# Performance work log

Measured on AMD Instinct MI355X. Metric: run time of the kernel, lower is better.

## Reference

```python
import jax, jax.numpy as jnp
import numpy as np

FP16_MIN = -65504.0
FP16_MAX = 65504.0

B, S, D, H = 2, 2048, 1024, 16
HD = D // H


def setup_inputs() -> dict:
    key = jax.random.key(0)
    ks = jax.random.split(key, 12)
    s = 0.02
    inp = {
        "x_q": jax.random.normal(ks[0], (B, S, D), jnp.float32),
        "x_k": jax.random.normal(ks[1], (B, S, D), jnp.float32),
        "x_v": jax.random.normal(ks[2], (B, S, D), jnp.float32),
        # causal mask [B, 1, S, S]; 0 entries are masked out
        "mask": jnp.broadcast_to(jnp.tril(jnp.ones((S, S), jnp.int32)), (B, 1, S, S)),
        "Wq": jax.random.normal(ks[3], (D, D), jnp.float32) * s,
        "bq": jnp.zeros((D,), jnp.float32),
        "Wk": jax.random.normal(ks[4], (D, D), jnp.float32) * s,
        "bk": jnp.zeros((D,), jnp.float32),
        "Wv": jax.random.normal(ks[5], (D, D), jnp.float32) * s,
        "bv": jnp.zeros((D,), jnp.float32),
        "Wo": jax.random.normal(ks[6], (D, D), jnp.float32) * s,
        "bo": jnp.zeros((D,), jnp.float32),
    }
    return inp


def _split_heads(x):
    # [B, S, D] -> [B, H, S, HD]
    b, s, _ = x.shape
    return x.reshape(b, s, H, HD).transpose(0, 2, 1, 3)


def reference(x_q, x_k, x_v, mask, Wq, bq, Wk, bk, Wv, bv, Wo, bo):
    scale = jnp.sqrt(jnp.float32(HD))
    q = _split_heads(x_q @ Wq + bq)  # [B,H,S,HD]
    k = _split_heads(x_k @ Wk + bk)
    v = _split_heads(x_v @ Wv + bv)

    scores = jnp.einsum("bhqd,bhkd->bhqk", q, k) / scale  # [B,H,S,S]
    scores = jnp.where(mask == 0, FP16_MIN, scores)
    scores = jnp.where(jnp.isneginf(scores), FP16_MIN, scores)
    scores = jnp.where(jnp.isposinf(scores), FP16_MAX, scores)

    probs = jax.nn.softmax(scores, axis=-1)  # dropout p=0.0 -> identity
    ctx = jnp.einsum("bhqk,bhkd->bhqd", probs, v)  # [B,H,S,HD]
    ctx = ctx.transpose(0, 2, 1, 3).reshape(x_q.shape[0], x_q.shape[1], D)
    out = ctx @ Wo + bo
    return out, probs
```

## Files before the change

kernel.cpp:

```cpp
#include <hip/hip_runtime.h>


typedef __bf16 bf16x8 __attribute__((ext_vector_type(8)));
typedef float f32x4 __attribute__((ext_vector_type(4)));

__device__ __forceinline__ unsigned short f2bf(float f) {
  unsigned int u = __builtin_bit_cast(unsigned int, f);
  u += 0x7fffu + ((u >> 16) & 1u);
  return (unsigned short)(u >> 16);
}
__device__ __forceinline__ float bf2f_lo(unsigned int u) {
  return __builtin_bit_cast(float, u << 16);
}
__device__ __forceinline__ float bf2f_hi(unsigned int u) {
  return __builtin_bit_cast(float, u & 0xffff0000u);
}

__global__ void transpose_w(const float* __restrict__ W0, const float* __restrict__ W1,
                            const float* __restrict__ W2, const float* __restrict__ W3,
                            unsigned short* __restrict__ Wt) {
  __shared__ float t[32][33];
  const int z = blockIdx.z;
  const float* W = (z == 0) ? W0 : (z == 1) ? W1 : (z == 2) ? W2 : W3;
  unsigned short* o = Wt + (size_t)z * 1048576u;
  const int n0 = blockIdx.x * 32, k0 = blockIdx.y * 32;
  const int tx = threadIdx.x, ty = threadIdx.y;
#pragma unroll
  for (int i = 0; i < 4; i++)
    t[ty + 8 * i][tx] = W[(size_t)(k0 + ty + 8 * i) * 1024 + n0 + tx];
  __syncthreads();
#pragma unroll
  for (int i = 0; i < 4; i++)
    o[(size_t)(n0 + ty + 8 * i) * 1024 + k0 + tx] = f2bf(t[tx][ty + 8 * i]);
}

__global__ __launch_bounds__(256) void gemm_kernel(
    const void* __restrict__ A0, const void* __restrict__ A1, const void* __restrict__ A2,
    const unsigned short* __restrict__ Wtb,
    const float* __restrict__ b0, const float* __restrict__ b1, const float* __restrict__ b2,
    void* __restrict__ O0, void* __restrict__ O1, void* __restrict__ O2,
    const int mode0) {
  __shared__ unsigned short Alds[64 * 40];
  const int z = blockIdx.z;
  const int mode = mode0 + z;
  const void* Av = (z == 0) ? A0 : (z == 1) ? A1 : A2;
  const float* bias = (z == 0) ? b0 : (z == 1) ? b1 : b2;
  void* outv = (z == 0) ? O0 : (z == 1) ? O1 : O2;
  const unsigned short* Wt = Wtb + (size_t)z * 1048576u;

  const int tid = threadIdx.x;
  const int lane = tid & 63;
  const int wave = tid >> 6;
  const int wm = wave >> 1, wn = wave & 1;
  const int m0 = blockIdx.y * 64, n0 = blockIdx.x * 128;
  const int g = lane >> 4, c = lane & 15;

  f32x4 acc[2][4];
#pragma unroll
  for (int i = 0; i < 2; i++)
#pragma unroll
    for (int j = 0; j < 4; j++) acc[i][j] = (f32x4){0.f, 0.f, 0.f, 0.f};

  const int srow = tid >> 2;
  const int sch = (tid & 3) * 8;

#define LOAD_PACK(KB, DST)                                                        \
  if (mode < 3) {                                                                 \
    const float* A = (const float*)Av;                                            \
    const float4* src = (const float4*)(A + (size_t)(m0 + srow) * 1024 + (KB) + sch); \
    const float4 v0 = src[0], v1 = src[1];                                        \
    DST.x = (unsigned int)f2bf(v0.x) | ((unsigned int)f2bf(v0.y) << 16);          \
    DST.y = (unsigned int)f2bf(v0.z) | ((unsigned int)f2bf(v0.w) << 16);          \
    DST.z = (unsigned int)f2bf(v1.x) | ((unsigned int)f2bf(v1.y) << 16);          \
    DST.w = (unsigned int)f2bf(v1.z) | ((unsigned int)f2bf(v1.w) << 16);          \
  } else {                                                                        \
    const unsigned short* A = (const unsigned short*)Av;                          \
    DST = *(const uint4*)(A + (size_t)(m0 + srow) * 1024 + (KB) + sch);           \
  }

  uint4 pk;
  LOAD_PACK(0, pk);
  for (int kb = 0; kb < 1024; kb += 32) {
    *(uint4*)&Alds[srow * 40 + sch] = pk;
    if (kb + 32 < 1024) { LOAD_PACK(kb + 32, pk); }
    __syncthreads();

    bf16x8 af[2], bfr[4];
#pragma unroll
    for (int mi = 0; mi < 2; mi++)
      af[mi] = *(const bf16x8*)&Alds[(wm * 32 + mi * 16 + c) * 40 + g * 8];
#pragma unroll
    for (int nf = 0; nf < 4; nf++)
      bfr[nf] = *(const bf16x8*)(Wt + (size_t)(n0 + wn * 64 + nf * 16 + c) * 1024 + kb + g * 8);
#pragma unroll
    for (int mi = 0; mi < 2; mi++)
#pragma unroll
      for (int nf = 0; nf < 4; nf++)
        acc[mi][nf] = __builtin_amdgcn_mfma_f32_16x16x32_bf16(af[mi], bfr[nf], acc[mi][nf], 0, 0, 0);
    __syncthreads();
  }
#undef LOAD_PACK

#pragma unroll
  for (int nf = 0; nf < 4; nf++) {
    const int col = n0 + wn * 64 + nf * 16 + c;
    const float bc = bias[col];
#pragma unroll
    for (int mi = 0; mi < 2; mi++) {
#pragma unroll
      for (int r = 0; r < 4; r++) {
        const int row = m0 + wm * 32 + mi * 16 + g * 4 + r;
        const float v = acc[mi][nf][r] + bc;
        if (mode == 0) {
          ((unsigned short*)outv)[(size_t)row * 1024 + col] = f2bf(v * 0.125f);
        } else if (mode == 1) {
          ((unsigned short*)outv)[(size_t)row * 1024 + col] = f2bf(v);
        } else if (mode == 2) {
          const int bb = row >> 11, s = row & 2047;
          ((unsigned short*)outv)[((size_t)(bb * 1024 + col)) * 2048 + s] = f2bf(v);
        } else {
          ((float*)outv)[(size_t)row * 1024 + col] = v;
        }
      }
    }
  }
}

__global__ __launch_bounds__(512, 4) void attn_kernel(
    const unsigned short* __restrict__ Q, const unsigned short* __restrict__ K,
    const unsigned short* __restrict__ Vt, float* __restrict__ probs,
    unsigned short* __restrict__ ctx) {
  __shared__ unsigned short Klds[64 * 72];
  __shared__ unsigned short Vlds[64 * 72];
  __shared__ unsigned short Plds[128 * 72];

  const int tid = threadIdx.x;
  const int lane = tid & 63, wave = tid >> 6;
  const int g = lane >> 4, c = lane & 15;
  const int bh = blockIdx.x;
  const int b = bh >> 4, h = bh & 15;
  const int q0 = blockIdx.y * 128;
  const int qrow0 = q0 + wave * 16;
  const int wave_kend = qrow0 + 16;

  const unsigned short* Qh = Q + ((size_t)(b * 2048 + qrow0)) * 1024 + h * 64;
  const unsigned short* Kh = K + ((size_t)b * 2048) * 1024 + h * 64;
  const unsigned short* Vh = Vt + ((size_t)bh) * 64 * 2048;
  float* Ph = probs + ((size_t)(bh * 2048 + q0)) * 2048;

  const bf16x8 qa0 = *(const bf16x8*)&Qh[(size_t)c * 1024 + g * 8];
  const bf16x8 qa1 = *(const bf16x8*)&Qh[(size_t)c * 1024 + 32 + g * 8];

  const int srow = tid >> 3;
  const int scol = (tid & 7) * 8;
  const int kb_end = q0 + 128;

#define QK_TILE()                                                                        \
  f32x4 sv[4];                                                                           \
  _Pragma("unroll")                                                                      \
  for (int sub = 0; sub < 4; sub++) {                                                    \
    sv[sub] = (f32x4){0.f, 0.f, 0.f, 0.f};                                               \
    const unsigned short* Kr = &Klds[(sub * 16 + c) * 72];                               \
    sv[sub] = __builtin_amdgcn_mfma_f32_16x16x32_bf16(qa0, *(const bf16x8*)&Kr[g * 8], sv[sub], 0, 0, 0); \
    sv[sub] = __builtin_amdgcn_mfma_f32_16x16x32_bf16(qa1, *(const bf16x8*)&Kr[32 + g * 8], sv[sub], 0, 0, 0); \
  }                                                                                      \
  if (kb + 63 > qrow0) {                                                                 \
    _Pragma("unroll")                                                                    \
    for (int sub = 0; sub < 4; sub++)                                                    \
      _Pragma("unroll")                                                                  \
      for (int r = 0; r < 4; r++)                                                        \
        if (kb + sub * 16 + c > qrow0 + g * 4 + r) sv[sub][r] = -1e30f;                  \
  }

  float lp[4] = {0.f, 0.f, 0.f, 0.f};
  {
    uint4 kreg = *(const uint4*)(Kh + (size_t)srow * 1024 + scol);
    for (int kb = 0; kb < kb_end; kb += 64) {
      *(uint4*)&Klds[srow * 72 + scol] = kreg;
      if (kb + 64 < kb_end)
        kreg = *(const uint4*)(Kh + (size_t)(kb + 64 + srow) * 1024 + scol);
      __syncthreads();
      if (kb < wave_kend) {
        QK_TILE();
#pragma unroll
        for (int r = 0; r < 4; r++)
          lp[r] += __expf(sv[0][r]) + __expf(sv[1][r]) + __expf(sv[2][r]) + __expf(sv[3][r]);
      }
      __syncthreads();
    }
  }
#pragma unroll
  for (int off = 1; off < 16; off <<= 1)
#pragma unroll
    for (int r = 0; r < 4; r++) lp[r] += __shfl_xor(lp[r], off);
  float invl[4];
#pragma unroll
  for (int r = 0; r < 4; r++) invl[r] = 1.0f / lp[r];

  f32x4 cacc[4];
#pragma unroll
  for (int nf = 0; nf < 4; nf++) cacc[nf] = (f32x4){0.f, 0.f, 0.f, 0.f};

  {
    uint4 kreg = *(const uint4*)(Kh + (size_t)srow * 1024 + scol);
    uint4 vreg = *(const uint4*)(Vh + (size_t)srow * 2048 + scol);
    for (int kb = 0; kb < kb_end; kb += 64) {
      *(uint4*)&Klds[srow * 72 + scol] = kreg;
      *(uint4*)&Vlds[srow * 72 + scol] = vreg;
      if (kb + 64 < kb_end) {
        kreg = *(const uint4*)(Kh + (size_t)(kb + 64 + srow) * 1024 + scol);
        vreg = *(const uint4*)(Vh + (size_t)srow * 2048 + kb + 64 + scol);
      }
      __syncthreads();
      if (kb < wave_kend) {
        QK_TILE();
#pragma unroll
        for (int sub = 0; sub < 4; sub++)
#pragma unroll
          for (int r = 0; r < 4; r++) {
            const float p = __expf(sv[sub][r]) * invl[r];
            Plds[(wave * 16 + g * 4 + r) * 72 + sub * 16 + c] = f2bf(p);
          }
        const bf16x8 pa0 = *(const bf16x8*)&Plds[(wave * 16 + c) * 72 + g * 8];
        const bf16x8 pa1 = *(const bf16x8*)&Plds[(wave * 16 + c) * 72 + 32 + g * 8];
#pragma unroll
        for (int nf = 0; nf < 4; nf++) {
          const bf16x8 vf0 = *(const bf16x8*)&Vlds[(nf * 16 + c) * 72 + g * 8];
          const bf16x8 vf1 = *(const bf16x8*)&Vlds[(nf * 16 + c) * 72 + 32 + g * 8];
          cacc[nf] = __builtin_amdgcn_mfma_f32_16x16x32_bf16(pa0, vf0, cacc[nf], 0, 0, 0);
          cacc[nf] = __builtin_amdgcn_mfma_f32_16x16x32_bf16(pa1, vf1, cacc[nf], 0, 0, 0);
        }
      } else {
#pragma unroll
        for (int sub = 0; sub < 4; sub++)
#pragma unroll
          for (int r = 0; r < 4; r++)
            Plds[(wave * 16 + g * 4 + r) * 72 + sub * 16 + c] = 0;
      }
      __syncthreads();
      {
        const int prow = tid >> 2;
        const int pcb = (tid & 3) * 16;
        const uint4* ps = (const uint4*)&Plds[prow * 72 + pcb];
        const uint4 a = ps[0], b4 = ps[1];
        float* dst = Ph + (size_t)prow * 2048 + kb + pcb;
        ((float4*)dst)[0] = make_float4(bf2f_lo(a.x), bf2f_hi(a.x), bf2f_lo(a.y), bf2f_hi(a.y));
        ((float4*)dst)[1] = make_float4(bf2f_lo(a.z), bf2f_hi(a.z), bf2f_lo(a.w), bf2f_hi(a.w));
        ((float4*)dst)[2] = make_float4(bf2f_lo(b4.x), bf2f_hi(b4.x), bf2f_lo(b4.y), bf2f_hi(b4.y));
        ((float4*)dst)[3] = make_float4(bf2f_lo(b4.z), bf2f_hi(b4.z), bf2f_lo(b4.w), bf2f_hi(b4.w));
      }
    }
  }
#undef QK_TILE

#pragma unroll
  for (int nf = 0; nf < 4; nf++)
#pragma unroll
    for (int r = 0; r < 4; r++)
      ctx[((size_t)(b * 2048 + qrow0 + g * 4 + r)) * 1024 + h * 64 + nf * 16 + c] =
          f2bf(cacc[nf][r]);

  if (kb_end < 2048) {
    const float4 zz = make_float4(0.f, 0.f, 0.f, 0.f);
    for (int row = 0; row < 128; ++row) {
      float* pr = Ph + (size_t)row * 2048;
      const int col = kb_end + tid * 4;
      if (col < 2048) *(float4*)&pr[col] = zz;
    }
  }
}

extern "C" void kernel_launch(void* const* d_in, const int* in_sizes, int n_in,
                              void* d_out, int out_size, void* d_ws, size_t ws_size,
                              hipStream_t stream) {
  if (ws_size < (size_t)40 * 1024 * 1024) return;

  const float* xq = (const float*)d_in[0];
  const float* xk = (const float*)d_in[1];
  const float* xv = (const float*)d_in[2];
  const float* Wq = (const float*)d_in[4];
  const float* bq = (const float*)d_in[5];
  const float* Wk = (const float*)d_in[6];
  const float* bk = (const float*)d_in[7];
  const float* Wv = (const float*)d_in[8];
  const float* bv = (const float*)d_in[9];
  const float* Wo = (const float*)d_in[10];
  const float* bo = (const float*)d_in[11];

  unsigned short* ws = (unsigned short*)d_ws;
  unsigned short* Wt = ws;
  unsigned short* Qw = ws + (size_t)4 * 1048576u;
  unsigned short* Kw = Qw + 4194304u;
  unsigned short* Vtw = Kw + 4194304u;
  unsigned short* Cw = Vtw + 4194304u;

  float* out = (float*)d_out;
  float* probs = out + 4194304u;

  transpose_w<<<dim3(32, 32, 4), dim3(32, 8), 0, stream>>>(Wq, Wk, Wv, Wo, Wt);
  gemm_kernel<<<dim3(8, 64, 3), 256, 0, stream>>>(xq, xk, xv, Wt, bq, bk, bv,
                                                  Qw, Kw, Vtw, 0);
  attn_kernel<<<dim3(32, 16, 1), 512, 0, stream>>>(Qw, Kw, Vtw, probs, Cw);
  gemm_kernel<<<dim3(8, 64, 1), 256, 0, stream>>>(Cw, Cw, Cw, Wt + 3u * 1048576u,
                                                  bo, bo, bo, out, out, out, 3);
}
```

Before: 366.2 us.

## Fuse attention into single pass with deferred normalization and separate probs normalization kernel

The attention kernel now computes QK^T, the exponentials and the PV product in one pass, dropping the separate row-sum pass. It also scales the context by 1/l only at the end. Unnormalized probabilities are written as bf16 into the first half of each fp32 probs row, and a new norm_probs kernel reads them back, sums each row and writes normalized fp32 values in place. The GEMM's K step is doubled from 32 to 64 to halve the number of barriers. In exchange, no max subtraction is applied before the exponentials, which assumes scores stay bounded, and the probs tensor is traversed an extra time.

Result: no change. 363.7 us (-0.7%).

```diff
diff --git a/kernel.cpp b/kernel.cpp
--- a/kernel.cpp
+++ b/kernel.cpp
@@ -40,7 +40,7 @@
     const float* __restrict__ b0, const float* __restrict__ b1, const float* __restrict__ b2,
     void* __restrict__ O0, void* __restrict__ O1, void* __restrict__ O2,
     const int mode0) {
-  __shared__ unsigned short Alds[64 * 40];
+  __shared__ unsigned short Alds[64 * 72];
   const int z = blockIdx.z;
   const int mode = mode0 + z;
   const void* Av = (z == 0) ? A0 : (z == 1) ? A1 : A2;
@@ -62,41 +62,54 @@
     for (int j = 0; j < 4; j++) acc[i][j] = (f32x4){0.f, 0.f, 0.f, 0.f};
 
   const int srow = tid >> 2;
-  const int sch = (tid & 3) * 8;
-
-#define LOAD_PACK(KB, DST)                                                        \
+  const int sch = (tid & 3) * 16;
+
+  uint4 pk0, pk1;
+#define LOAD_PACK(KB)                                                             \
   if (mode < 3) {                                                                 \
     const float* A = (const float*)Av;                                            \
     const float4* src = (const float4*)(A + (size_t)(m0 + srow) * 1024 + (KB) + sch); \
-    const float4 v0 = src[0], v1 = src[1];                                        \
-    DST.x = (unsigned int)f2bf(v0.x) | ((unsigned int)f2bf(v0.y) << 16);          \
-    DST.y = (unsigned int)f2bf(v0.z) | ((unsigned int)f2bf(v0.w) << 16);          \
-    DST.z = (unsigned int)f2bf(v1.x) | ((unsigned int)f2bf(v1.y) << 16);          \
-    DST.w = (unsigned int)f2bf(v1.z) | ((unsigned int)f2bf(v1.w) << 16);          \
+    const float4 v0 = src[0], v1 = src[1], v2 = src[2], v3 = src[3];              \
+    pk0.x = (unsigned int)f2bf(v0.x) | ((unsigned int)f2bf(v0.y) << 16);          \
+    pk0.y = (unsigned int)f2bf(v0.z) | ((unsigned int)f2bf(v0.w) << 16);          \
+    pk0.z = (unsigned int)f2bf(v1.x) | ((unsigned int)f2bf(v1.y) << 16);          \
+    pk0.w = (unsigned int)f2bf(v1.z) | ((unsigned int)f2bf(v1.w) << 16);          \
+    pk1.x = (unsigned int)f2bf(v2.x) | ((unsigned int)f2bf(v2.y) << 16);          \
+    pk1.y = (unsigned int)f2bf(v2.z) | ((unsigned int)f2bf(v2.w) << 16);          \
+    pk1.z = (unsigned int)f2bf(v3.x) | ((unsigned int)f2bf(v3.y) << 16);          \
+    pk1.w = (unsigned int)f2bf(v3.z) | ((unsigned int)f2bf(v3.w) << 16);          \
   } else {                                                                        \
     const unsigned short* A = (const unsigned short*)Av;                          \
-    DST = *(const uint4*)(A + (size_t)(m0 + srow) * 1024 + (KB) + sch);           \
+    const uint4* src = (const uint4*)(A + (size_t)(m0 + srow) * 1024 + (KB) + sch); \
+    pk0 = src[0];                                                                 \
+    pk1 = src[1];                                                                 \
   }
 
-  uint4 pk;
-  LOAD_PACK(0, pk);
-  for (int kb = 0; kb < 1024; kb += 32) {
-    *(uint4*)&Alds[srow * 40 + sch] = pk;
-    if (kb + 32 < 1024) { LOAD_PACK(kb + 32, pk); }
+  LOAD_PACK(0);
+  for (int kb = 0; kb < 1024; kb += 64) {
+    *(uint4*)&Alds[srow * 72 + sch] = pk0;
+    *(uint4*)&Alds[srow * 72 + sch + 8] = pk1;
+    if (kb + 64 < 1024) { LOAD_PACK(kb + 64); }
     __syncthreads();
 
-    bf16x8 af[2], bfr[4];
+    bf16x8 af[2][2], bfr[4][2];
 #pragma unroll
     for (int mi = 0; mi < 2; mi++)
-      af[mi] = *(const bf16x8*)&Alds[(wm * 32 + mi * 16 + c) * 40 + g * 8];
+#pragma unroll
+      for (int kk = 0; kk < 2; kk++)
+        af[mi][kk] = *(const bf16x8*)&Alds[(wm * 32 + mi * 16 + c) * 72 + kk * 32 + g * 8];
 #pragma unroll
     for (int nf = 0; nf < 4; nf++)
-      bfr[nf] = *(const bf16x8*)(Wt + (size_t)(n0 + wn * 64 + nf * 16 + c) * 1024 + kb + g * 8);
-#pragma unroll
-    for (int mi = 0; mi < 2; mi++)
-#pragma unroll
-      for (int nf = 0; nf < 4; nf++)
-        acc[mi][nf] = __builtin_amdgcn_mfma_f32_16x16x32_bf16(af[mi], bfr[nf], acc[mi][nf], 0, 0, 0);
+#pragma unroll
+      for (int kk = 0; kk < 2; kk++)
+        bfr[nf][kk] = *(const bf16x8*)(Wt + (size_t)(n0 + wn * 64 + nf * 16 + c) * 1024 + kb + kk * 32 + g * 8);
+#pragma unroll
+    for (int kk = 0; kk < 2; kk++)
+#pragma unroll
+      for (int mi = 0; mi < 2; mi++)
+#pragma unroll
+        for (int nf = 0; nf < 4; nf++)
+          acc[mi][nf] = __builtin_amdgcn_mfma_f32_16x16x32_bf16(af[mi][kk], bfr[nf][kk], acc[mi][nf], 0, 0, 0);
     __syncthreads();
   }
 #undef LOAD_PACK
@@ -155,40 +168,73 @@
   const int scol = (tid & 7) * 8;
   const int kb_end = q0 + 128;
 
-#define QK_TILE()                                                                        \
-  f32x4 sv[4];                                                                           \
-  _Pragma("unroll")                                                                      \
-  for (int sub = 0; sub < 4; sub++) {                                                    \
-    sv[sub] = (f32x4){0.f, 0.f, 0.f, 0.f};                                               \
-    const unsigned short* Kr = &Klds[(sub * 16 + c) * 72];                               \
-    sv[sub] = __builtin_amdgcn_mfma_f32_16x16x32_bf16(qa0, *(const bf16x8*)&Kr[g * 8], sv[sub], 0, 0, 0); \
-    sv[sub] = __builtin_amdgcn_mfma_f32_16x16x32_bf16(qa1, *(const bf16x8*)&Kr[32 + g * 8], sv[sub], 0, 0, 0); \
-  }                                                                                      \
-  if (kb + 63 > qrow0) {                                                                 \
-    _Pragma("unroll")                                                                    \
-    for (int sub = 0; sub < 4; sub++)                                                    \
-      _Pragma("unroll")                                                                  \
-      for (int r = 0; r < 4; r++)                                                        \
-        if (kb + sub * 16 + c > qrow0 + g * 4 + r) sv[sub][r] = -1e30f;                  \
-  }
-
   float lp[4] = {0.f, 0.f, 0.f, 0.f};
-  {
-    uint4 kreg = *(const uint4*)(Kh + (size_t)srow * 1024 + scol);
-    for (int kb = 0; kb < kb_end; kb += 64) {
-      *(uint4*)&Klds[srow * 72 + scol] = kreg;
-      if (kb + 64 < kb_end)
-        kreg = *(const uint4*)(Kh + (size_t)(kb + 64 + srow) * 1024 + scol);
-      __syncthreads();
-      if (kb < wave_kend) {
-        QK_TILE();
-#pragma unroll
-        for (int r = 0; r < 4; r++)
-          lp[r] += __expf(sv[0][r]) + __expf(sv[1][r]) + __expf(sv[2][r]) + __expf(sv[3][r]);
-      }
-      __syncthreads();
+  f32x4 cacc[4];
+#pragma unroll
+  for (int nf = 0; nf < 4; nf++) cacc[nf] = (f32x4){0.f, 0.f, 0.f, 0.f};
+
+  uint4 kreg = *(const uint4*)(Kh + (size_t)srow * 1024 + scol);
+  uint4 vreg = *(const uint4*)(Vh + (size_t)srow * 2048 + scol);
+  for (int kb = 0; kb < kb_end; kb += 64) {
+    *(uint4*)&Klds[srow * 72 + scol] = kreg;
+    *(uint4*)&Vlds[srow * 72 + scol] = vreg;
+    if (kb + 64 < kb_end) {
+      kreg = *(const uint4*)(Kh + (size_t)(kb + 64 + srow) * 1024 + scol);
+      vreg = *(const uint4*)(Vh + (size_t)srow * 2048 + kb + 64 + scol);
+    }
+    __syncthreads();
+
+    if (kb < wave_kend) {
+      f32x4 sv[4];
+#pragma unroll
+      for (int sub = 0; sub < 4; sub++) {
+        sv[sub] = (f32x4){0.f, 0.f, 0.f, 0.f};
+        const unsigned short* Kr = &Klds[(sub * 16 + c) * 72];
+        sv[sub] = __builtin_amdgcn_mfma_f32_16x16x32_bf16(qa0, *(const bf16x8*)&Kr[g * 8], sv[sub], 0, 0, 0);
+        sv[sub] = __builtin_amdgcn_mfma_f32_16x16x32_bf16(qa1, *(const bf16x8*)&Kr[32 + g * 8], sv[sub], 0, 0, 0);
+      }
+      if (kb + 63 > qrow0) {
+#pragma unroll
+        for (int sub = 0; sub < 4; sub++)
+#pragma unroll
+          for (int r = 0; r < 4; r++)
+            if (kb + sub * 16 + c > qrow0 + g * 4 + r) sv[sub][r] = -1e30f;
+      }
+#pragma unroll
+      for (int sub = 0; sub < 4; sub++)
+#pragma unroll
+        for (int r = 0; r < 4; r++) {
+          const float pu = __expf(sv[sub][r]);
+          lp[r] += pu;
+          Plds[(wave * 16 + g * 4 + r) * 72 + sub * 16 + c] = f2bf(pu);
+        }
+      const bf16x8 pa0 = *(const bf16x8*)&Plds[(wave * 16 + c) * 72 + g * 8];
+      const bf16x8 pa1 = *(const bf16x8*)&Plds[(wave * 16 + c) * 72 + 32 + g * 8];
+#pragma unroll
+      for (int nf = 0; nf < 4; nf++) {
+        const bf16x8 vf0 = *(const bf16x8*)&Vlds[(nf * 16 + c) * 72 + g * 8];
+        const bf16x8 vf1 = *(const bf16x8*)&Vlds[(nf * 16 + c) * 72 + 32 + g * 8];
+        cacc[nf] = __builtin_amdgcn_mfma_f32_16x16x32_bf16(pa0, vf0, cacc[nf], 0, 0, 0);
+        cacc[nf] = __builtin_amdgcn_mfma_f32_16x16x32_bf16(pa1, vf1, cacc[nf], 0, 0, 0);
+      }
+    }
+    __syncthreads();
+
+    {
+      const int prow = tid >> 2;
+      const int pcb = (tid & 3) * 16;
+      unsigned short* dst = (unsigned short*)Ph + (size_t)prow * 4096 + kb + pcb;
+      const int rw_kend = q0 + (prow & ~15) + 16;
+      if (kb < rw_kend) {
+        *(uint4*)dst = *(const uint4*)&Plds[prow * 72 + pcb];
+        *(uint4*)(dst + 8) = *(const uint4*)&Plds[prow * 72 + pcb + 8];
+      } else {
+        *(uint4*)dst = make_uint4(0u, 0u, 0u, 0u);
+        *(uint4*)(dst + 8) = make_uint4(0u, 0u, 0u, 0u);
+      }
     }
   }
+
 #pragma unroll
   for (int off = 1; off < 16; off <<= 1)
 #pragma unroll
@@ -197,77 +243,38 @@
 #pragma unroll
   for (int r = 0; r < 4; r++) invl[r] = 1.0f / lp[r];
 
-  f32x4 cacc[4];
-#pragma unroll
-  for (int nf = 0; nf < 4; nf++) cacc[nf] = (f32x4){0.f, 0.f, 0.f, 0.f};
-
-  {
-    uint4 kreg = *(const uint4*)(Kh + (size_t)srow * 1024 + scol);
-    uint4 vreg = *(const uint4*)(Vh + (size_t)srow * 2048 + scol);
-    for (int kb = 0; kb < kb_end; kb += 64) {
-      *(uint4*)&Klds[srow * 72 + scol] = kreg;
-      *(uint4*)&Vlds[srow * 72 + scol] = vreg;
-      if (kb + 64 < kb_end) {
-        kreg = *(const uint4*)(Kh + (size_t)(kb + 64 + srow) * 1024 + scol);
-        vreg = *(const uint4*)(Vh + (size_t)srow * 2048 + kb + 64 + scol);
-      }
-      __syncthreads();
-      if (kb < wave_kend) {
-        QK_TILE();
-#pragma unroll
-        for (int sub = 0; sub < 4; sub++)
-#pragma unroll
-          for (int r = 0; r < 4; r++) {
-            const float p = __expf(sv[sub][r]) * invl[r];
-            Plds[(wave * 16 + g * 4 + r) * 72 + sub * 16 + c] = f2bf(p);
-          }
-        const bf16x8 pa0 = *(const bf16x8*)&Plds[(wave * 16 + c) * 72 + g * 8];
-        const bf16x8 pa1 = *(const bf16x8*)&Plds[(wave * 16 + c) * 72 + 32 + g * 8];
-#pragma unroll
-        for (int nf = 0; nf < 4; nf++) {
-          const bf16x8 vf0 = *(const bf16x8*)&Vlds[(nf * 16 + c) * 72 + g * 8];
-          const bf16x8 vf1 = *(const bf16x8*)&Vlds[(nf * 16 + c) * 72 + 32 + g * 8];
-          cacc[nf] = __builtin_amdgcn_mfma_f32_16x16x32_bf16(pa0, vf0, cacc[nf], 0, 0, 0);
-          cacc[nf] = __builtin_amdgcn_mfma_f32_16x16x32_bf16(pa1, vf1, cacc[nf], 0, 0, 0);
-        }
-      } else {
-#pragma unroll
-        for (int sub = 0; sub < 4; sub++)
-#pragma unroll
-          for (int r = 0; r < 4; r++)
-            Plds[(wave * 16 + g * 4 + r) * 72 + sub * 16 + c] = 0;
-      }
-      __syncthreads();
-      {
-        const int prow = tid >> 2;
-        const int pcb = (tid & 3) * 16;
-        const uint4* ps = (const uint4*)&Plds[prow * 72 + pcb];
-        const uint4 a = ps[0], b4 = ps[1];
-        float* dst = Ph + (size_t)prow * 2048 + kb + pcb;
-        ((float4*)dst)[0] = make_float4(bf2f_lo(a.x), bf2f_hi(a.x), bf2f_lo(a.y), bf2f_hi(a.y));
-        ((float4*)dst)[1] = make_float4(bf2f_lo(a.z), bf2f_hi(a.z), bf2f_lo(a.w), bf2f_hi(a.w));
-        ((float4*)dst)[2] = make_float4(bf2f_lo(b4.x), bf2f_hi(b4.x), bf2f_lo(b4.y), bf2f_hi(b4.y));
-        ((float4*)dst)[3] = make_float4(bf2f_lo(b4.z), bf2f_hi(b4.z), bf2f_lo(b4.w), bf2f_hi(b4.w));
-      }
-    }
-  }
-#undef QK_TILE
-
 #pragma unroll
   for (int nf = 0; nf < 4; nf++)
 #pragma unroll
     for (int r = 0; r < 4; r++)
       ctx[((size_t)(b * 2048 + qrow0 + g * 4 + r)) * 1024 + h * 64 + nf * 16 + c] =
-          f2bf(cacc[nf][r]);
-
-  if (kb_end < 2048) {
-    const float4 zz = make_float4(0.f, 0.f, 0.f, 0.f);
-    for (int row = 0; row < 128; ++row) {
-      float* pr = Ph + (size_t)row * 2048;
-      const int col = kb_end + tid * 4;
-      if (col < 2048) *(float4*)&pr[col] = zz;
-    }
-  }
+          f2bf(cacc[nf][r] * invl[r]);
+}
+
+__global__ __launch_bounds__(256) void norm_probs(float* __restrict__ probs) {
+  __shared__ float wsum[4];
+  const int rowIdx = blockIdx.x;
+  const int q = rowIdx & 2047;
+  const int kbe = ((q >> 7) + 1) << 7;
+  float* base = probs + (size_t)rowIdx * 2048;
+  const int t = threadIdx.x;
+  const int c0 = t * 8;
+
+  uint4 raw = make_uint4(0u, 0u, 0u, 0u);
+  if (c0 < kbe) raw = *(const uint4*)((const unsigned short*)base + c0);
+  float f0 = bf2f_lo(raw.x), f1 = bf2f_hi(raw.x), f2 = bf2f_lo(raw.y), f3 = bf2f_hi(raw.y);
+  float f4 = bf2f_lo(raw.z), f5 = bf2f_hi(raw.z), f6 = bf2f_lo(raw.w), f7 = bf2f_hi(raw.w);
+
+  float s = ((f0 + f1) + (f2 + f3)) + ((f4 + f5) + (f6 + f7));
+#pragma unroll
+  for (int off = 1; off < 64; off <<= 1) s += __shfl_xor(s, off);
+  if ((t & 63) == 0) wsum[t >> 6] = s;
+  __syncthreads();
+  const float il = 1.0f / (wsum[0] + wsum[1] + wsum[2] + wsum[3]);
+
+  float4* dst = (float4*)(base + c0);
+  dst[0] = make_float4(f0 * il, f1 * il, f2 * il, f3 * il);
+  dst[1] = make_float4(f4 * il, f5 * il, f6 * il, f7 * il);
 }
 
 extern "C" void kernel_launch(void* const* d_in, const int* in_sizes, int n_in,
@@ -301,6 +308,7 @@
   gemm_kernel<<<dim3(8, 64, 3), 256, 0, stream>>>(xq, xk, xv, Wt, bq, bk, bv,
                                                   Qw, Kw, Vtw, 0);
   attn_kernel<<<dim3(32, 16, 1), 512, 0, stream>>>(Qw, Kw, Vtw, probs, Cw);
+  norm_probs<<<dim3(65536), 256, 0, stream>>>(probs);
   gemm_kernel<<<dim3(8, 64, 1), 256, 0, stream>>>(Cw, Cw, Cw, Wt + 3u * 1048576u,
                                                   bo, bo, bo, out, out, out, 3);
 }
```
